# Kernel optimization log

Measured on AMD Instinct MI355X. Metric: run time of the kernel, lower is better.

Reference implementation:

```python
import jax, jax.numpy as jnp
import numpy as np

FP8_MAX = 448.0
FP8_HI_PREC_MAX = 224.0
UNC_THRESH = 0.1
EPS = 1e-08


def setup_inputs() -> dict:
    key = jax.random.key(0)
    k1, k2, k3 = jax.random.split(key, 3)
    B, S, H, D, M = 1, 4096, 32, 128, 4096
    return {
        "k": jax.random.normal(k1, (B, S, H, D), dtype=jnp.float32),
        "v": jax.random.normal(k2, (B, S, H, D), dtype=jnp.float32),
        "uncertainty": jax.random.uniform(k3, (B, S), dtype=jnp.float32),
        "k_cache": jnp.zeros((H, M, D), dtype=jnp.float32),
        "v_cache": jnp.zeros((H, M, D), dtype=jnp.float32),
        "k_scales": jnp.ones((H, M), dtype=jnp.float32),
        "v_scales": jnp.ones((H, M), dtype=jnp.float32),
        "current_pos": 0,
    }


def reference(k, v, uncertainty, k_cache, v_cache, k_scales, v_scales, current_pos):
    # k, v: [1, S, H, D]; caches: [H, M, D]; scales: [H, M]
    H, M, D = k_cache.shape
    S = k.shape[1]
    pos = (current_pos + jnp.arange(S)) % M  # circular-buffer write positions

    kt = k[0]  # [S, H, D]
    vt = v[0]

    # per-token fp8 divisor: high-precision range when uncertain
    div = jnp.where(uncertainty[0] > UNC_THRESH, FP8_HI_PREC_MAX, FP8_MAX)  # [S]

    # per-token amax over all heads and dims -> scalar scale per token
    k_s = jnp.maximum(jnp.max(jnp.abs(kt), axis=(1, 2)) / div, EPS)  # [S]
    v_s = jnp.maximum(jnp.max(jnp.abs(vt), axis=(1, 2)) / div, EPS)

    kq = jnp.clip(kt / k_s[:, None, None], -FP8_MAX, FP8_MAX)  # [S, H, D]
    vq = jnp.clip(vt / v_s[:, None, None], -FP8_MAX, FP8_MAX)

    # scatter-append into circular buffer ([H, S, D] layout for cache writes)
    new_k_cache = k_cache.at[:, pos].set(jnp.swapaxes(kq, 0, 1))
    new_v_cache = v_cache.at[:, pos].set(jnp.swapaxes(vq, 0, 1))
    new_k_scales = k_scales.at[:, pos].set(jnp.broadcast_to(k_s, (H, S)))
    new_v_scales = v_scales.at[:, pos].set(jnp.broadcast_to(v_s, (H, S)))
    return (new_k_cache, new_v_cache, new_k_scales, new_v_scales)
```

## Files before the change

kernel.cpp:

```cpp
#include <hip/hip_runtime.h>

#define HH 32
#define DD 128
#define MM 4096
#define ROW_F4 1024
#define D_F4   32
#define TPB    4

typedef float v4f __attribute__((ext_vector_type(4)));

__device__ __forceinline__ void gl_lds16(const v4f* g, v4f* l) {
    __builtin_amdgcn_global_load_lds(
        (const __attribute__((address_space(1))) unsigned int*)g,
        (__attribute__((address_space(3))) unsigned int*)l,
        16, 0, 0);
}

__device__ __forceinline__ int src_token(int m, int cpm, int S) {
    int s0 = m - cpm; if (s0 < 0) s0 += MM;
    return (s0 < S) ? (s0 + MM * ((S - 1 - s0) / MM)) : -1;
}

__global__ __launch_bounds__(256)
void teleport_fused(const float* __restrict__ kin,
                    const float* __restrict__ vin,
                    const float* __restrict__ unc,
                    const float* __restrict__ kc_in,
                    const float* __restrict__ vc_in,
                    const float* __restrict__ ksc_in,
                    const float* __restrict__ vsc_in,
                    const int*   __restrict__ cur_pos,
                    float* __restrict__ kc_out,
                    float* __restrict__ vc_out,
                    float* __restrict__ ksc_out,
                    float* __restrict__ vsc_out,
                    int S)
{
    __shared__ v4f   sh[TPB * ROW_F4];
    __shared__ float sc_l[TPB];

    const int t    = threadIdx.x;
    const int lane = t & 63;
    const int wv   = t >> 6;
    const int b    = blockIdx.x;
    const int isV  = b >> 10;
    const int mb   = (b & 1023) * TPB;

    const float* in_  = isV ? vin : kin;
    const float* cin  = isV ? vc_in : kc_in;
    float*       cout = isV ? vc_out : kc_out;
    const float* sin_ = isV ? vsc_in  : ksc_in;
    float*       sout = isV ? vsc_out : ksc_out;

    int cp  = *cur_pos;
    int cpm = cp % MM; if (cpm < 0) cpm += MM;

    const int m = mb + wv;
    const int s = src_token(m, cpm, S);
    if (s >= 0) {
        const v4f* src = reinterpret_cast<const v4f*>(in_) + (size_t)s * ROW_F4;
        #pragma unroll
        for (int c = 0; c < 16; ++c)
            gl_lds16(src + c * 64 + lane, sh + wv * ROW_F4 + c * 64);
    } else {
        const v4f* cb = reinterpret_cast<const v4f*>(cin);
        #pragma unroll
        for (int c = 0; c < 16; ++c) {
            int f4 = c * 64 + lane;
            gl_lds16(cb + (size_t)(f4 >> 5) * (MM * D_F4) + (size_t)m * D_F4 + (f4 & 31),
                     sh + wv * ROW_F4 + c * 64);
        }
    }
    asm volatile("s_waitcnt vmcnt(0)" ::: "memory");

    if (s >= 0) {
        float am = 0.0f;
        #pragma unroll
        for (int c = 0; c < 16; ++c) {
            v4f a = sh[wv * ROW_F4 + c * 64 + lane];
            am = fmaxf(am, fmaxf(fmaxf(fabsf(a.x), fabsf(a.y)),
                                 fmaxf(fabsf(a.z), fabsf(a.w))));
        }
        #pragma unroll
        for (int off = 32; off > 0; off >>= 1)
            am = fmaxf(am, __shfl_xor(am, off, 64));
        if (lane == 0) {
            const float u   = unc[s];
            const float div = (u > 0.1f) ? 224.0f : 448.0f;
            sc_l[wv] = fmaxf(am / div, 1e-8f);
        }
    }
    __syncthreads();

    const int ml   = (t >> 5) & (TPB - 1);
    const int d4   = t & 31;
    const int hoff = t >> 7;
    const int mq   = mb + ml;
    const int sq   = src_token(mq, cpm, S);
    const float r  = (sq >= 0) ? (1.0f / sc_l[ml]) : 1.0f;

    v4f* coutv = reinterpret_cast<v4f*>(cout);
    #pragma unroll
    for (int i = 0; i < 16; ++i) {
        const int h = 2 * i + hoff;
        v4f a = sh[ml * ROW_F4 + h * D_F4 + d4];
        v4f q;
        if (sq >= 0) {
            q.x = fminf(fmaxf(a.x * r, -448.0f), 448.0f);
            q.y = fminf(fmaxf(a.y * r, -448.0f), 448.0f);
            q.z = fminf(fmaxf(a.z * r, -448.0f), 448.0f);
            q.w = fminf(fmaxf(a.w * r, -448.0f), 448.0f);
        } else {
            q = a;
        }
        coutv[(size_t)h * (MM * D_F4) + (size_t)mq * D_F4 + d4] = q;
    }

    if (t < 128) {
        const int h   = t >> 2;
        const int mll = t & 3;
        const int msc = mb + mll;
        const int ss  = src_token(msc, cpm, S);
        sout[h * MM + msc] = (ss >= 0) ? sc_l[mll] : sin_[h * MM + msc];
    }
}

extern "C" void kernel_launch(void* const* d_in, const int* in_sizes, int n_in,
                              void* d_out, int out_size, void* d_ws, size_t ws_size,
                              hipStream_t stream) {
    const float* kin = (const float*)d_in[0];
    const float* vin = (const float*)d_in[1];
    const float* unc = (const float*)d_in[2];
    const float* kc  = (const float*)d_in[3];
    const float* vc  = (const float*)d_in[4];
    const float* ksc = (const float*)d_in[5];
    const float* vsc = (const float*)d_in[6];
    const int*   cp  = (const int*)d_in[7];
    const int S = in_sizes[2];

    float* out  = (float*)d_out;
    float* kco  = out;
    float* vco  = kco + (size_t)HH * MM * DD;
    float* ksco = vco + (size_t)HH * MM * DD;
    float* vsco = ksco + (size_t)HH * MM;

    teleport_fused<<<2 * (MM / TPB), 256, 0, stream>>>(
        kin, vin, unc, kc, vc, ksc, vsc, cp, kco, vco, ksco, vsco, S);
}
```

Before: 49.67 us.

## Process 32 tokens per block with two-pass global reads instead of LDS staging

Result: slower. 63.15 us (+27.1%).

```diff
diff --git a/kernel.cpp b/kernel.cpp
--- a/kernel.cpp
+++ b/kernel.cpp
@@ -5,46 +5,40 @@
 #define MM 4096
 #define ROW_F4 1024
 #define D_F4   32
-#define TPB    4
+#define CHUNK  32
 
 typedef float v4f __attribute__((ext_vector_type(4)));
 
-__device__ __forceinline__ void gl_lds16(const v4f* g, v4f* l) {
-    __builtin_amdgcn_global_load_lds(
-        (const __attribute__((address_space(1))) unsigned int*)g,
-        (__attribute__((address_space(3))) unsigned int*)l,
-        16, 0, 0);
+__device__ __forceinline__ int src_token(int m, int cpm, int S) {
+    int s0 = m - cpm; if (s0 < 0) s0 += MM;
+    return (s0 < S) ? (s0 + MM * ((S - 1 - s0) >> 12)) : -1;
 }
 
-__device__ __forceinline__ int src_token(int m, int cpm, int S) {
-    int s0 = m - cpm; if (s0 < 0) s0 += MM;
-    return (s0 < S) ? (s0 + MM * ((S - 1 - s0) / MM)) : -1;
-}
-
-__global__ __launch_bounds__(256)
-void teleport_fused(const float* __restrict__ kin,
-                    const float* __restrict__ vin,
-                    const float* __restrict__ unc,
-                    const float* __restrict__ kc_in,
-                    const float* __restrict__ vc_in,
-                    const float* __restrict__ ksc_in,
-                    const float* __restrict__ vsc_in,
-                    const int*   __restrict__ cur_pos,
-                    float* __restrict__ kc_out,
-                    float* __restrict__ vc_out,
-                    float* __restrict__ ksc_out,
-                    float* __restrict__ vsc_out,
-                    int S)
+__global__ __launch_bounds__(256, 1)
+void teleport_fused2(const float* __restrict__ kin,
+                     const float* __restrict__ vin,
+                     const float* __restrict__ unc,
+                     const float* __restrict__ kc_in,
+                     const float* __restrict__ vc_in,
+                     const float* __restrict__ ksc_in,
+                     const float* __restrict__ vsc_in,
+                     const int*   __restrict__ cur_pos,
+                     float* __restrict__ kc_out,
+                     float* __restrict__ vc_out,
+                     float* __restrict__ ksc_out,
+                     float* __restrict__ vsc_out,
+                     int S)
 {
-    __shared__ v4f   sh[TPB * ROW_F4];
-    __shared__ float sc_l[TPB];
+    __shared__ float sc_l[CHUNK];
+    __shared__ float rc_l[CHUNK];
+    __shared__ int   s_l [CHUNK];
 
     const int t    = threadIdx.x;
     const int lane = t & 63;
     const int wv   = t >> 6;
     const int b    = blockIdx.x;
-    const int isV  = b >> 10;
-    const int mb   = (b & 1023) * TPB;
+    const int isV  = b & 1;
+    const int mb   = (b >> 1) * CHUNK;
 
     const float* in_  = isV ? vin : kin;
     const float* cin  = isV ? vc_in : kc_in;
@@ -55,73 +49,81 @@
     int cp  = *cur_pos;
     int cpm = cp % MM; if (cpm < 0) cpm += MM;
 
-    const int m = mb + wv;
-    const int s = src_token(m, cpm, S);
-    if (s >= 0) {
-        const v4f* src = reinterpret_cast<const v4f*>(in_) + (size_t)s * ROW_F4;
-        #pragma unroll
-        for (int c = 0; c < 16; ++c)
-            gl_lds16(src + c * 64 + lane, sh + wv * ROW_F4 + c * 64);
-    } else {
-        const v4f* cb = reinterpret_cast<const v4f*>(cin);
-        #pragma unroll
-        for (int c = 0; c < 16; ++c) {
-            int f4 = c * 64 + lane;
-            gl_lds16(cb + (size_t)(f4 >> 5) * (MM * D_F4) + (size_t)m * D_F4 + (f4 & 31),
-                     sh + wv * ROW_F4 + c * 64);
-        }
-    }
-    asm volatile("s_waitcnt vmcnt(0)" ::: "memory");
-
-    if (s >= 0) {
-        float am = 0.0f;
-        #pragma unroll
-        for (int c = 0; c < 16; ++c) {
-            v4f a = sh[wv * ROW_F4 + c * 64 + lane];
-            am = fmaxf(am, fmaxf(fmaxf(fabsf(a.x), fabsf(a.y)),
-                                 fmaxf(fabsf(a.z), fabsf(a.w))));
-        }
-        #pragma unroll
-        for (int off = 32; off > 0; off >>= 1)
-            am = fmaxf(am, __shfl_xor(am, off, 64));
-        if (lane == 0) {
-            const float u   = unc[s];
-            const float div = (u > 0.1f) ? 224.0f : 448.0f;
-            sc_l[wv] = fmaxf(am / div, 1e-8f);
+    for (int j = 0; j < 8; ++j) {
+        const int ml = wv + 4 * j;
+        const int m  = mb + ml;
+        const int s  = src_token(m, cpm, S);
+        if (s >= 0) {
+            const v4f* src = reinterpret_cast<const v4f*>(in_) + (size_t)s * ROW_F4;
+            float am0 = 0.0f, am1 = 0.0f;
+            #pragma unroll
+            for (int c = 0; c < 16; c += 2) {
+                v4f a = src[c * 64 + lane];
+                v4f d = src[(c + 1) * 64 + lane];
+                am0 = fmaxf(am0, fmaxf(fmaxf(fabsf(a.x), fabsf(a.y)),
+                                       fmaxf(fabsf(a.z), fabsf(a.w))));
+                am1 = fmaxf(am1, fmaxf(fmaxf(fabsf(d.x), fabsf(d.y)),
+                                       fmaxf(fabsf(d.z), fabsf(d.w))));
+            }
+            float am = fmaxf(am0, am1);
+            #pragma unroll
+            for (int off = 32; off > 0; off >>= 1)
+                am = fmaxf(am, __shfl_xor(am, off, 64));
+            if (lane == 0) {
+                const float u   = unc[s];
+                const float div = (u > 0.1f) ? 224.0f : 448.0f;
+                const float sc  = fmaxf(am / div, 1e-8f);
+                sc_l[ml] = sc;
+                rc_l[ml] = 1.0f / sc;
+                s_l [ml] = s;
+            }
+        } else if (lane == 0) {
+            s_l[ml] = -1;
         }
     }
     __syncthreads();
 
-    const int ml   = (t >> 5) & (TPB - 1);
-    const int d4   = t & 31;
-    const int hoff = t >> 7;
-    const int mq   = mb + ml;
-    const int sq   = src_token(mq, cpm, S);
-    const float r  = (sq >= 0) ? (1.0f / sc_l[ml]) : 1.0f;
+    const int d4  = lane & 31;
+    const int hi2 = lane >> 5;
+    v4f* coutv = reinterpret_cast<v4f*>(cout);
+    const v4f* cinv = reinterpret_cast<const v4f*>(cin);
+    const v4f* inv  = reinterpret_cast<const v4f*>(in_);
 
-    v4f* coutv = reinterpret_cast<v4f*>(cout);
-    #pragma unroll
-    for (int i = 0; i < 16; ++i) {
-        const int h = 2 * i + hoff;
-        v4f a = sh[ml * ROW_F4 + h * D_F4 + d4];
-        v4f q;
-        if (sq >= 0) {
-            q.x = fminf(fmaxf(a.x * r, -448.0f), 448.0f);
-            q.y = fminf(fmaxf(a.y * r, -448.0f), 448.0f);
-            q.z = fminf(fmaxf(a.z * r, -448.0f), 448.0f);
-            q.w = fminf(fmaxf(a.w * r, -448.0f), 448.0f);
-        } else {
-            q = a;
+    for (int jj = 0; jj < 8; ++jj) {
+        const int h = 8 * wv + jj;
+        v4f* ob = coutv + (size_t)h * (MM * D_F4) + (size_t)mb * D_F4;
+
+        v4f a[16];
+        #pragma unroll
+        for (int i = 0; i < 16; ++i) {
+            const int ml = 2 * i + hi2;
+            const int s  = s_l[ml];
+            a[i] = (s >= 0)
+                 ? inv [(size_t)s * ROW_F4 + h * D_F4 + d4]
+                 : cinv[(size_t)h * (MM * D_F4) + (size_t)(mb + ml) * D_F4 + d4];
         }
-        coutv[(size_t)h * (MM * D_F4) + (size_t)mq * D_F4 + d4] = q;
+        #pragma unroll
+        for (int i = 0; i < 16; ++i) {
+            const int ml = 2 * i + hi2;
+            v4f q = a[i];
+            if (s_l[ml] >= 0) {
+                const float r = rc_l[ml];
+                q.x = fminf(fmaxf(q.x * r, -448.0f), 448.0f);
+                q.y = fminf(fmaxf(q.y * r, -448.0f), 448.0f);
+                q.z = fminf(fmaxf(q.z * r, -448.0f), 448.0f);
+                q.w = fminf(fmaxf(q.w * r, -448.0f), 448.0f);
+            }
+            ob[ml * D_F4 + d4] = q;
+        }
     }
 
-    if (t < 128) {
-        const int h   = t >> 2;
-        const int mll = t & 3;
-        const int msc = mb + mll;
-        const int ss  = src_token(msc, cpm, S);
-        sout[h * MM + msc] = (ss >= 0) ? sc_l[mll] : sin_[h * MM + msc];
+    #pragma unroll
+    for (int q = 0; q < 4; ++q) {
+        const int idx = q * 256 + t;
+        const int h   = idx >> 5;
+        const int ml  = idx & 31;
+        const int m   = mb + ml;
+        sout[h * MM + m] = (s_l[ml] >= 0) ? sc_l[ml] : sin_[h * MM + m];
     }
 }
 
@@ -144,6 +146,6 @@
     float* ksco = vco + (size_t)HH * MM * DD;
     float* vsco = ksco + (size_t)HH * MM;
 
-    teleport_fused<<<2 * (MM / TPB), 256, 0, stream>>>(
+    teleport_fused2<<<2 * (MM / CHUNK), 256, 0, stream>>>(
         kin, vin, unc, kc, vc, ksc, vsc, cp, kco, vco, ksco, vsco, S);
 }
```
